# Optimization experiments

Hardware: AMD Instinct MI355X
Metric: run time of the kernel (lower is better)

The kernel has to match this reference:

```python
import jax, jax.numpy as jnp
import numpy as np
from jax import lax

# pywt db4 reconstruction low-pass (scaling) coefficients
_REC_LO = np.array([
    0.23037781330885523, 0.7148465705525415, 0.6308807679295904,
    -0.02798376941698385, -0.18703481171888114, 0.030841381835986965,
    0.032883011666982945, -0.010597401784997278], dtype=np.float64)
_DEC_LO = _REC_LO[::-1].copy()                       # pywt dec_lo = reversed rec_lo
_DEC_HI = (_REC_LO * ((-1.0) ** (np.arange(8) + 1)))  # pywt qmf: dec_hi[k] = (-1)^(k+1) rec_lo[k]
FLEN = 8
LEVEL = 4


def _dwt_level(x):
    """One pywt dwt level, mode='symmetric'. x: [N, n] -> (cA, cD) each [N, floor((n+7)/2)]."""
    # half-sample symmetric extension by FLEN-1 on each side, then drop the first
    # sample so a stride-2 VALID conv lands on pywt's odd-indexed outputs.
    ext = jnp.pad(x, ((0, 0), (FLEN - 1, FLEN - 1)), mode='symmetric')[:, 1:]
    # pywt performs true convolution with dec filters -> flip kernels for XLA correlation
    k = jnp.stack([_DEC_LO[::-1], _DEC_HI[::-1]]).astype(x.dtype)[:, None, :]  # [2,1,8]
    y = lax.conv_general_dilated(ext[:, None, :], k, window_strides=(2,),
                                 padding='VALID',
                                 dimension_numbers=('NCH', 'OIH', 'NCH'))  # [N,2,out]
    return y[:, 0], y[:, 1]


def setup_inputs() -> dict:
    key = jax.random.key(0)
    x = jax.random.normal(key, (64, 32, 8192), dtype=jnp.float32)
    return {"x": x}


def reference(x) -> jnp.ndarray:
    """Batched pywt.wavedec(x, 'db4', mode='symmetric', level=4), coeffs concatenated.
    x: [B, C, L] -> [B, C, wavelet_len] with order [cA4, cD4, cD3, cD2, cD1]."""
    B, C, L = x.shape
    a = x.reshape(B * C, L)
    details = []
    for _ in range(LEVEL):
        a, d = _dwt_level(a)
        details.append(d)
    coeffs = jnp.concatenate([a] + details[::-1], axis=-1)  # [B*C, total]
    return coeffs.reshape(B, C, -1)
```

## Files before the change

kernel.cpp:

```cpp
#include <hip/hip_runtime.h>

#define NT 256

constexpr int LPAD = 8;
constexpr int L0 = 8192;
constexpr int N1 = 4099;
constexpr int N2 = 2053;
constexpr int N3 = 1030;
constexpr int N4 = 518;
constexpr int ROW_OUT = N4 + N4 + N3 + N2 + N1;

constexpr float GLO[8] = {
    0.23037781330885523f,  0.7148465705525415f,   0.6308807679295904f,
   -0.02798376941698385f, -0.18703481171888114f,  0.030841381835986965f,
    0.032883011666982945f, -0.010597401784997278f };
constexpr float GHI[8] = {
   -0.010597401784997278f, -0.032883011666982945f, 0.030841381835986965f,
    0.18703481171888114f,  -0.02798376941698385f,  -0.6308807679295904f,
    0.7148465705525415f,   -0.23037781330885523f };

__device__ __forceinline__ void dwt_level_lds(const float* __restrict__ in, int nout,
                                              float* __restrict__ lo_out,
                                              float* __restrict__ hi_out, int tid)
{
    for (int i = tid; i < nout; i += NT) {
        const float* p = in + 2 * i + 2;
        float lo = 0.f, hi = 0.f;
#pragma unroll
        for (int j = 0; j < 8; ++j) {
            float v = p[j];
            lo = fmaf(GLO[j], v, lo);
            hi = fmaf(GHI[j], v, hi);
        }
        lo_out[i] = lo;
        hi_out[i] = hi;
    }
}

__global__ __launch_bounds__(NT) void wavedec4_db4(const float* __restrict__ x,
                                                   float* __restrict__ out)
{
    __shared__ float bufA[LPAD + L0 + 8];
    __shared__ float bufB[LPAD + N1 + 8];
    const int tid = threadIdx.x;
    const size_t row = blockIdx.x;
    const float* __restrict__ xr = x + row * (size_t)L0;
    float* __restrict__ outr = out + row * (size_t)ROW_OUT;

    const float4* x4 = (const float4*)xr;
    float4* a4 = (float4*)(bufA + LPAD);
    for (int i = tid; i < L0 / 4; i += NT) a4[i] = x4[i];
    if (tid < 7) {
        bufA[LPAD - 1 - tid] = xr[tid];
        bufA[LPAD + L0 + tid] = xr[L0 - 1 - tid];
    }
    __syncthreads();

    dwt_level_lds(bufA, N1, bufB + LPAD, outr + (N4 + N4 + N3 + N2), tid);
    __syncthreads();
    if (tid < 7) {
        bufB[LPAD - 1 - tid] = bufB[LPAD + tid];
        bufB[LPAD + N1 + tid] = bufB[LPAD + N1 - 1 - tid];
    }
    __syncthreads();

    dwt_level_lds(bufB, N2, bufA + LPAD, outr + (N4 + N4 + N3), tid);
    __syncthreads();
    if (tid < 7) {
        bufA[LPAD - 1 - tid] = bufA[LPAD + tid];
        bufA[LPAD + N2 + tid] = bufA[LPAD + N2 - 1 - tid];
    }
    __syncthreads();

    dwt_level_lds(bufA, N3, bufB + LPAD, outr + (N4 + N4), tid);
    __syncthreads();
    if (tid < 7) {
        bufB[LPAD - 1 - tid] = bufB[LPAD + tid];
        bufB[LPAD + N3 + tid] = bufB[LPAD + N3 - 1 - tid];
    }
    __syncthreads();

    dwt_level_lds(bufB, N4, outr, outr + N4, tid);
}

extern "C" void kernel_launch(void* const* d_in, const int* in_sizes, int n_in,
                              void* d_out, int out_size, void* d_ws, size_t ws_size,
                              hipStream_t stream) {
    const float* x = (const float*)d_in[0];
    float* out = (float*)d_out;
    const int rows = in_sizes[0] / L0;
    wavedec4_db4<<<dim3(rows), dim3(NT), 0, stream>>>(x, out);
}
```

Baseline: 117.5 us.

## Store signal as even/odd polyphase arrays in LDS to avoid strided reads

Splits each level's signal into separate even and odd LDS arrays so the stride-2 filter taps become unit-stride reads across threads. This removes LDS bank conflicts from the strided access pattern. Low-pass outputs are scattered by parity into the next level's even/odd buffers, and the symmetric boundary padding is rebuilt per array. The padding index logic is more intricate and the parity-split writes are less regular.

```diff
diff --git a/kernel.cpp b/kernel.cpp
--- a/kernel.cpp
+++ b/kernel.cpp
@@ -2,7 +2,6 @@
 
 #define NT 256
 
-constexpr int LPAD = 8;
 constexpr int L0 = 8192;
 constexpr int N1 = 4099;
 constexpr int N2 = 2053;
@@ -19,68 +18,90 @@
     0.18703481171888114f,  -0.02798376941698385f,  -0.6308807679295904f,
     0.7148465705525415f,   -0.23037781330885523f };
 
-__device__ __forceinline__ void dwt_level_lds(const float* __restrict__ in, int nout,
-                                              float* __restrict__ lo_out,
-                                              float* __restrict__ hi_out, int tid)
+__device__ __forceinline__ void set_pads(float* __restrict__ e, float* __restrict__ o,
+                                         int n, int nE, int nO, int nout, int tid)
+{
+    if (tid < 4) {
+        if (tid < 3) {
+            e[-1 - tid] = o[tid];
+            o[-1 - tid] = e[tid];
+        }
+        if (tid < nout - nE) e[nE + tid] = o[n - 1 - nE - tid];
+        if (tid < nout - nO) o[nO + tid] = e[n - 1 - nO - tid];
+    }
+}
+
+template <bool LAST>
+__device__ __forceinline__ void dwt_level_split(const float* __restrict__ e,
+                                                const float* __restrict__ o,
+                                                int nout,
+                                                float* __restrict__ eN,
+                                                float* __restrict__ oN,
+                                                float* __restrict__ loG,
+                                                float* __restrict__ hiG, int tid)
 {
     for (int i = tid; i < nout; i += NT) {
-        const float* p = in + 2 * i + 2;
+        const float* pe = e + i - 3;
+        const float* po = o + i - 3;
         float lo = 0.f, hi = 0.f;
 #pragma unroll
-        for (int j = 0; j < 8; ++j) {
-            float v = p[j];
-            lo = fmaf(GLO[j], v, lo);
-            hi = fmaf(GHI[j], v, hi);
+        for (int m = 0; m < 4; ++m) {
+            float ve = pe[m];
+            float vo = po[m];
+            lo = fmaf(GLO[2 * m], ve, lo);
+            lo = fmaf(GLO[2 * m + 1], vo, lo);
+            hi = fmaf(GHI[2 * m], ve, hi);
+            hi = fmaf(GHI[2 * m + 1], vo, hi);
         }
-        lo_out[i] = lo;
-        hi_out[i] = hi;
+        hiG[i] = hi;
+        if (LAST) {
+            loG[i] = lo;
+        } else {
+            float* t = (i & 1) ? oN : eN;
+            t[i >> 1] = lo;
+        }
     }
 }
 
 __global__ __launch_bounds__(NT) void wavedec4_db4(const float* __restrict__ x,
                                                    float* __restrict__ out)
 {
-    __shared__ float bufA[LPAD + L0 + 8];
-    __shared__ float bufB[LPAD + N1 + 8];
+    __shared__ __align__(16) float eA[4 + 4096 + 4], oA[4 + 4096 + 4];
+    __shared__ __align__(16) float eB[4 + 2050 + 4], oB[4 + 2050 + 4];
     const int tid = threadIdx.x;
-    const size_t row = blockIdx.x;
-    const float* __restrict__ xr = x + row * (size_t)L0;
-    float* __restrict__ outr = out + row * (size_t)ROW_OUT;
+    const float* __restrict__ xr = x + blockIdx.x * (size_t)L0;
+    float* __restrict__ outr = out + blockIdx.x * (size_t)ROW_OUT;
+    float* E0 = eA + 4; float* O0 = oA + 4;
+    float* E1 = eB + 4; float* O1 = oB + 4;
 
     const float4* x4 = (const float4*)xr;
-    float4* a4 = (float4*)(bufA + LPAD);
-    for (int i = tid; i < L0 / 4; i += NT) a4[i] = x4[i];
-    if (tid < 7) {
-        bufA[LPAD - 1 - tid] = xr[tid];
-        bufA[LPAD + L0 + tid] = xr[L0 - 1 - tid];
+    float2* e2 = (float2*)E0;
+    float2* o2 = (float2*)O0;
+    for (int idx = tid; idx < L0 / 4; idx += NT) {
+        float4 v = x4[idx];
+        e2[idx] = make_float2(v.x, v.z);
+        o2[idx] = make_float2(v.y, v.w);
     }
     __syncthreads();
-
-    dwt_level_lds(bufA, N1, bufB + LPAD, outr + (N4 + N4 + N3 + N2), tid);
-    __syncthreads();
-    if (tid < 7) {
-        bufB[LPAD - 1 - tid] = bufB[LPAD + tid];
-        bufB[LPAD + N1 + tid] = bufB[LPAD + N1 - 1 - tid];
-    }
+    set_pads(E0, O0, L0, 4096, 4096, N1, tid);
     __syncthreads();
 
-    dwt_level_lds(bufB, N2, bufA + LPAD, outr + (N4 + N4 + N3), tid);
+    dwt_level_split<false>(E0, O0, N1, E1, O1, nullptr, outr + (N4 + N4 + N3 + N2), tid);
     __syncthreads();
-    if (tid < 7) {
-        bufA[LPAD - 1 - tid] = bufA[LPAD + tid];
-        bufA[LPAD + N2 + tid] = bufA[LPAD + N2 - 1 - tid];
-    }
+    set_pads(E1, O1, N1, 2050, 2049, N2, tid);
     __syncthreads();
 
-    dwt_level_lds(bufA, N3, bufB + LPAD, outr + (N4 + N4), tid);
+    dwt_level_split<false>(E1, O1, N2, E0, O0, nullptr, outr + (N4 + N4 + N3), tid);
     __syncthreads();
-    if (tid < 7) {
-        bufB[LPAD - 1 - tid] = bufB[LPAD + tid];
-        bufB[LPAD + N3 + tid] = bufB[LPAD + N3 - 1 - tid];
-    }
+    set_pads(E0, O0, N2, 1027, 1026, N3, tid);
     __syncthreads();
 
-    dwt_level_lds(bufB, N4, outr, outr + N4, tid);
+    dwt_level_split<false>(E0, O0, N3, E1, O1, nullptr, outr + (N4 + N4), tid);
+    __syncthreads();
+    set_pads(E1, O1, N3, 515, 515, N4, tid);
+    __syncthreads();
+
+    dwt_level_split<true>(E1, O1, N4, nullptr, nullptr, outr, outr + N4, tid);
 }
 
 extern "C" void kernel_launch(void* const* d_in, const int* in_sizes, int n_in,
```

Result: no change. 118.6 us (+0.9%).
